# Kernel tuning notes

Hardware: AMD Instinct MI355X
Metric: run time of the kernel (lower is better)

Reference implementation:

```python
import jax, jax.numpy as jnp
import numpy as np

EPS = 1e-08


def setup_inputs() -> dict:
    key = jax.random.key(0)
    k1, k2, k3 = jax.random.split(key, 3)
    b, c, s = 4, 128, 32
    oc, k = 128, 3
    x = jax.random.normal(k1, (b, c, s, s, s), dtype=jnp.float32)
    y = jax.random.normal(k2, (b, c), dtype=jnp.float32)
    weight = jax.random.normal(k3, (oc, c, k, k, k), dtype=jnp.float32)
    return {"x": x, "y": y, "weight": weight}


def reference(x, y, weight):
    b, c, h, w, d = x.shape
    oc, ic, kh, kw, kd = weight.shape
    # modulate: per-sample scale of input channels
    ws = weight[None] * y[:, None, :, None, None, None]  # (b, oc, ic, k, k, k)
    # demodulate
    demod = jax.lax.rsqrt(jnp.sum(jnp.square(ws), axis=(2, 3, 4, 5)) + EPS)  # (b, oc)
    ws = ws * demod[:, :, None, None, None, None]
    # grouped conv: fold batch into channels, groups=b
    xr = x.reshape(1, b * c, h, w, d)
    wr = ws.reshape(b * oc, ic, kh, kw, kd)
    # same padding for stride=1, dilation=1: (k-1)//2
    pad = (kh - 1) // 2
    out = jax.lax.conv_general_dilated(
        xr, wr,
        window_strides=(1, 1, 1),
        padding=[(pad, pad)] * 3,
        feature_group_count=b,
        dimension_numbers=("NCDHW", "OIDHW", "NCDHW"),
    )
    return out.reshape(b, oc, h, w, d)
```

## Files before the change

kernel.cpp:

```cpp
#include <hip/hip_runtime.h>
#include <hip/hip_bf16.h>

typedef __attribute__((ext_vector_type(8))) short bf16x8;
typedef __attribute__((ext_vector_type(4))) float f32x4;
typedef unsigned short u16;
typedef unsigned int u32;

#define NP 34
#define XT_BYTES ((size_t)4 * NP * NP * NP * 128 * 2)

__device__ __forceinline__ u16 f2bf(float f) {
  __hip_bfloat16 h = __float2bfloat16(f);
  return __builtin_bit_cast(u16, h);
}

__device__ __forceinline__ void gload_lds16(const u16* g, u16* l) {
  __builtin_amdgcn_global_load_lds(
      (const __attribute__((address_space(1))) u32*)g,
      (__attribute__((address_space(3))) u32*)l, 16, 0, 0);
}

#define WAITV(N) asm volatile("s_waitcnt vmcnt(" #N ")" ::: "memory")
#define BAR() do { __builtin_amdgcn_s_barrier(); asm volatile("" ::: "memory"); } while (0)

__global__ __launch_bounds__(128) void kmodw(const float* __restrict__ w,
                                             const float* __restrict__ y,
                                             u16* __restrict__ wmod) {
  const int oc = blockIdx.x, b = blockIdx.y;
  const int ic = threadIdx.x;
  const float* wp = w + (oc * 128 + ic) * 27;
  float wv[27];
  float s = 0.f;
#pragma unroll
  for (int t = 0; t < 27; ++t) { wv[t] = wp[t]; s += wv[t] * wv[t]; }
  const float yv = y[b * 128 + ic];
  float v = yv * yv * s;
#pragma unroll
  for (int m = 1; m < 64; m <<= 1) v += __shfl_xor(v, m);
  __shared__ float part[2];
  const int lane = ic & 63, wid = ic >> 6;
  if (lane == 0) part[wid] = v;
  __syncthreads();
  const float demod = rsqrtf(part[0] + part[1] + 1e-8f);
  const float sc = yv * demod;
#pragma unroll
  for (int t = 0; t < 27; ++t)
    wmod[((b * 27 + t) * 128 + oc) * 128 + ic] = f2bf(wv[t] * sc);
}

__global__ __launch_bounds__(128) void khalo(u16* __restrict__ xt) {
  const int zy = blockIdx.x, b = blockIdx.y;
  const int zz = zy / NP, yy = zy % NP;
  u16* row = xt + ((size_t)((b * NP + zz) * NP + yy) * NP) * 128;
  u32* wp = (u32*)row;
  if (zz == 0 || zz == NP - 1 || yy == 0 || yy == NP - 1) {
#pragma unroll
    for (int i = 0; i < 17; ++i) wp[i * 128 + threadIdx.x] = 0;
  } else {
    if (threadIdx.x < 64) wp[threadIdx.x] = 0;
    else ((u32*)(row + 33 * 128))[threadIdx.x - 64] = 0;
  }
}

__global__ __launch_bounds__(256) void kcastx(const float* __restrict__ x,
                                              u16* __restrict__ xt) {
  const int yq = blockIdx.x, z = blockIdx.y, b = blockIdx.z;
  const int tid = threadIdx.x;
  __shared__ u16 t[32 * 132];
  const float* xp = x + (size_t)b * 128 * 32768 + (z * 32 + yq) * 32;
#pragma unroll
  for (int p = 0; p < 16; ++p) {
    const int ic = p * 8 + (tid >> 5), xx = tid & 31;
    t[xx * 132 + ic] = f2bf(xp[(size_t)ic * 32768 + xx]);
  }
  __syncthreads();
  u16* xtb = xt + (((size_t)(b * NP + z + 1) * NP + (yq + 1)) * NP + 1) * 128;
#pragma unroll
  for (int p = 0; p < 4; ++p) {
    const int xx = p * 8 + (tid >> 5), icq = tid & 31;
    *(ushort4*)(xtb + (size_t)xx * 128 + icq * 4) = *(const ushort4*)&t[xx * 132 + icq * 4];
  }
}

__global__ __launch_bounds__(256, 2) void kconv(const u16* __restrict__ xt,
                                                const u16* __restrict__ wmod,
                                                float* __restrict__ out) {
  __shared__ __align__(16) u16 Alds[2][128 * 64];
  __shared__ __align__(16) u16 Blds[2][160 * 64];
  const int tid = threadIdx.x;
  const int lane = tid & 63, wid = tid >> 6;
  const int bsw = ((blockIdx.x & 7) << 7) + (blockIdx.x >> 3);
  const int yt = bsw & 7, z = (bsw >> 3) & 31, b = bsw >> 8;
  const int y0 = yt << 2;
  const int wm = wid >> 1, wn = wid & 1;

  const u16* xb = xt + (size_t)b * (NP * NP * NP) * 128;
  const u16* wb = wmod + (size_t)b * 27 * 16384;

  f32x4 acc[4][4];
#pragma unroll
  for (int i = 0; i < 4; ++i)
#pragma unroll
    for (int j = 0; j < 4; ++j) acc[i][j] = (f32x4){0.f, 0.f, 0.f, 0.f};

  auto stageA = [&](int tap, int h) {
    const u16* base = wb + tap * 16384 + (h << 6);
#pragma unroll
    for (int k = 0; k < 4; ++k) {
      const int s = (k << 8) + tid;
      const int oc = s >> 3, j = s & 7;
      gload_lds16(base + (oc << 7) + ((j ^ (oc & 7)) << 3),
                  &Alds[h][((k << 8) + (wid << 6)) << 3]);
    }
  };
  auto stageB = [&](int g) {
    const int dz = g / 3 - 1, dy = g % 3 - 1;
    const int pz = z + 1 + dz;
#pragma unroll
    for (int k = 0; k < 10; ++k) {
      const int h = (k >= 5) ? 1 : 0;
      const int k5 = (k >= 5) ? (k - 5) : k;
      const int s = (k5 << 8) + tid;
      const int r = s >> 3, j = s & 7;
      const int yy = r / 40;
      int px = r - yy * 40;
      px = px < 34 ? px : 33;
      const int py = y0 + yy + 1 + dy;
      gload_lds16(xb + ((size_t)(pz * NP + py) * NP + px) * 128 + (h << 6) +
                      ((j ^ (r & 7)) << 3),
                  &Blds[h][((k5 << 8) + (wid << 6)) << 3]);
    }
  };

#define COMPHALF(H, DXI)                                                     \
  {                                                                          \
    const u16* Ah = &Alds[H][0];                                             \
    const u16* Bh = &Blds[H][0];                                             \
    _Pragma("unroll") for (int kk = 0; kk < 2; ++kk) {                       \
      const int sg = (kk << 2) + (lane >> 4);                                \
      bf16x8 af[4], bv[4];                                                   \
      _Pragma("unroll") for (int m = 0; m < 4; ++m) {                        \
        const int row = (wm << 6) + (m << 4) + (lane & 15);                  \
        af[m] = *(const bf16x8*)&Ah[(row << 6) + ((sg ^ (row & 7)) << 3)];   \
      }                                                                      \
      _Pragma("unroll") for (int n = 0; n < 4; ++n) {                        \
        const int nn = (wn << 6) + (n << 4) + (lane & 15);                   \
        const int r = ((nn >> 5) * 40) + (nn & 31) + (DXI);                  \
        bv[n] = *(const bf16x8*)&Bh[(r << 6) + ((sg ^ (r & 7)) << 3)];       \
      }                                                                      \
      __builtin_amdgcn_s_setprio(1);                                         \
      _Pragma("unroll") for (int m = 0; m < 4; ++m)                          \
        _Pragma("unroll") for (int n = 0; n < 4; ++n)                        \
          acc[m][n] = __builtin_amdgcn_mfma_f32_16x16x32_bf16(               \
              af[m], bv[n], acc[m][n], 0, 0, 0);                             \
      __builtin_amdgcn_s_setprio(0);                                         \
    }                                                                        \
  }

  stageB(0);
  stageA(0, 0);
  stageA(0, 1);

  for (int g = 0; g < 9; ++g) {
    const int t = g * 3;
    WAITV(4); BAR(); COMPHALF(0, 0); BAR(); stageA(t + 1, 0);
    WAITV(4); BAR(); COMPHALF(1, 0); BAR(); stageA(t + 1, 1);
    WAITV(4); BAR(); COMPHALF(0, 1); BAR(); stageA(t + 2, 0);
    WAITV(4); BAR(); COMPHALF(1, 1); BAR(); stageA(t + 2, 1);
    WAITV(4); BAR(); COMPHALF(0, 2); BAR();
    if (g < 8) stageA(t + 3, 0);
    if (g < 8) {
      WAITV(4); BAR(); COMPHALF(1, 2); BAR();
      stageB(g + 1);
      stageA(t + 3, 1);
    } else {
      WAITV(0); BAR(); COMPHALF(1, 2);
    }
  }

  const int col = lane & 15, rg = lane >> 4;
#pragma unroll
  for (int m = 0; m < 4; ++m) {
    const int ocb = (wm << 6) + (m << 4) + (rg << 2);
#pragma unroll
    for (int n = 0; n < 4; ++n) {
      const int nn = (wn << 6) + (n << 4) + col;
      const int yy = nn >> 5, xx = nn & 31;
      float* op = out + ((size_t)(b * 128 + ocb) << 15) + (z << 10) +
                  ((y0 + yy) << 5) + xx;
#pragma unroll
      for (int r = 0; r < 4; ++r) op[(size_t)r << 15] = acc[m][n][r];
    }
  }
#undef COMPHALF
}

extern "C" void kernel_launch(void* const* d_in, const int* in_sizes, int n_in,
                              void* d_out, int out_size, void* d_ws, size_t ws_size,
                              hipStream_t stream) {
  const float* x = (const float*)d_in[0];
  const float* y = (const float*)d_in[1];
  const float* w = (const float*)d_in[2];
  float* out = (float*)d_out;
  u16* xt = (u16*)d_ws;
  u16* wmod = (u16*)((char*)d_ws + XT_BYTES);

  hipLaunchKernelGGL(khalo, dim3(NP * NP, 4), dim3(128), 0, stream, xt);
  hipLaunchKernelGGL(kmodw, dim3(128, 4), dim3(128), 0, stream, w, y, wmod);
  hipLaunchKernelGGL(kcastx, dim3(32, 32, 4), dim3(256), 0, stream, x, xt);
  hipLaunchKernelGGL(kconv, dim3(1024), dim3(256), 0, stream, xt, wmod, out);
}
```

Before: 144.2 us.

## Load conv activations directly from global into registers with larger per-block tile

Drops LDS staging of the input (B) tile; each wave now loads its B fragments straight from global memory into registers, double-buffered across the two K halves of every tap. The block tile doubles to 128 oc by 256 spatial positions (8 y rows), each wave covers all 128 output channels, and the grid halves to 512 blocks. This removes the LDS traffic and barriers for B and reuses the weight tile across more positions. In exchange, accumulator registers double, B reuse across the three dx taps now depends on the cache instead of LDS, and global load latency sits directly on the compute path.

After: 160.4 us. 1.11x slower.

```diff
diff --git a/kernel.cpp b/kernel.cpp
--- a/kernel.cpp
+++ b/kernel.cpp
@@ -85,114 +85,110 @@
 __global__ __launch_bounds__(256, 2) void kconv(const u16* __restrict__ xt,
                                                 const u16* __restrict__ wmod,
                                                 float* __restrict__ out) {
-  __shared__ __align__(16) u16 Alds[2][128 * 64];
-  __shared__ __align__(16) u16 Blds[2][160 * 64];
+  __shared__ __align__(16) u16 Asm[2][1024 * 8];
   const int tid = threadIdx.x;
-  const int lane = tid & 63, wid = tid >> 6;
-  const int bsw = ((blockIdx.x & 7) << 7) + (blockIdx.x >> 3);
-  const int yt = bsw & 7, z = (bsw >> 3) & 31, b = bsw >> 8;
-  const int y0 = yt << 2;
-  const int wm = wid >> 1, wn = wid & 1;
-
-  const u16* xb = xt + (size_t)b * (NP * NP * NP) * 128;
+  const int lane = tid & 63, wn = tid >> 6;
+  const int l15 = lane & 15, sg = lane >> 4;
+  const int bsw = ((blockIdx.x & 7) << 6) + (blockIdx.x >> 3);
+  const int yt = bsw & 3, z = (bsw >> 2) & 31, b = bsw >> 7;
+  const int y0 = yt << 3;
+
   const u16* wb = wmod + (size_t)b * 27 * 16384;
-
-  f32x4 acc[4][4];
-#pragma unroll
-  for (int i = 0; i < 4; ++i)
+  const char* xbp = (const char*)(xt + (size_t)b * (NP * NP * NP) * 128);
+
+  int bofs[4];
+#pragma unroll
+  for (int nf = 0; nf < 4; ++nf) {
+    const int yy = (wn << 1) + (nf >> 1);
+    const int xx = ((nf & 1) << 4) + l15;
+    bofs[nf] = (((z + 1) * NP + (y0 + yy + 1)) * NP + (xx + 1)) * 256 + (sg << 4);
+  }
+
+  f32x4 acc[8][4];
+#pragma unroll
+  for (int i = 0; i < 8; ++i)
 #pragma unroll
     for (int j = 0; j < 4; ++j) acc[i][j] = (f32x4){0.f, 0.f, 0.f, 0.f};
 
   auto stageA = [&](int tap, int h) {
-    const u16* base = wb + tap * 16384 + (h << 6);
 #pragma unroll
     for (int k = 0; k < 4; ++k) {
       const int s = (k << 8) + tid;
-      const int oc = s >> 3, j = s & 7;
-      gload_lds16(base + (oc << 7) + ((j ^ (oc & 7)) << 3),
-                  &Alds[h][((k << 8) + (wid << 6)) << 3]);
+      const int oc = s >> 3, jp = s & 7, jg = jp ^ (oc & 7);
+      gload_lds16(wb + tap * 16384 + (oc << 7) + (h << 6) + (jg << 3),
+                  &Asm[h][s << 3]);
     }
   };
-  auto stageB = [&](int g) {
-    const int dz = g / 3 - 1, dy = g % 3 - 1;
-    const int pz = z + 1 + dz;
-#pragma unroll
-    for (int k = 0; k < 10; ++k) {
-      const int h = (k >= 5) ? 1 : 0;
-      const int k5 = (k >= 5) ? (k - 5) : k;
-      const int s = (k5 << 8) + tid;
-      const int r = s >> 3, j = s & 7;
-      const int yy = r / 40;
-      int px = r - yy * 40;
-      px = px < 34 ? px : 33;
-      const int py = y0 + yy + 1 + dy;
-      gload_lds16(xb + ((size_t)(pz * NP + py) * NP + px) * 128 + (h << 6) +
-                      ((j ^ (r & 7)) << 3),
-                  &Blds[h][((k5 << 8) + (wid << 6)) << 3]);
-    }
+  auto loadB = [&](bf16x8* bv, int toff) {
+#pragma unroll
+    for (int nf = 0; nf < 4; ++nf)
+#pragma unroll
+      for (int kk = 0; kk < 2; ++kk)
+        bv[nf * 2 + kk] =
+            *(const bf16x8*)(xbp + (bofs[nf] + toff + (kk << 6)));
   };
 
-#define COMPHALF(H, DXI)                                                     \
+#define COMPUTE(PAR, BV)                                                     \
   {                                                                          \
-    const u16* Ah = &Alds[H][0];                                             \
-    const u16* Bh = &Blds[H][0];                                             \
     _Pragma("unroll") for (int kk = 0; kk < 2; ++kk) {                       \
-      const int sg = (kk << 2) + (lane >> 4);                                \
-      bf16x8 af[4], bv[4];                                                   \
-      _Pragma("unroll") for (int m = 0; m < 4; ++m) {                        \
-        const int row = (wm << 6) + (m << 4) + (lane & 15);                  \
-        af[m] = *(const bf16x8*)&Ah[(row << 6) + ((sg ^ (row & 7)) << 3)];   \
-      }                                                                      \
-      _Pragma("unroll") for (int n = 0; n < 4; ++n) {                        \
-        const int nn = (wn << 6) + (n << 4) + (lane & 15);                   \
-        const int r = ((nn >> 5) * 40) + (nn & 31) + (DXI);                  \
-        bv[n] = *(const bf16x8*)&Bh[(r << 6) + ((sg ^ (r & 7)) << 3)];       \
+      bf16x8 af[8];                                                          \
+      _Pragma("unroll") for (int m = 0; m < 8; ++m) {                        \
+        const int oc = (m << 4) + l15;                                       \
+        const int jp = ((kk << 2) + sg) ^ (oc & 7);                          \
+        af[m] = *(const bf16x8*)&Asm[PAR][(oc << 6) + (jp << 3)];            \
       }                                                                      \
       __builtin_amdgcn_s_setprio(1);                                         \
-      _Pragma("unroll") for (int m = 0; m < 4; ++m)                          \
-        _Pragma("unroll") for (int n = 0; n < 4; ++n)                        \
-          acc[m][n] = __builtin_amdgcn_mfma_f32_16x16x32_bf16(               \
-              af[m], bv[n], acc[m][n], 0, 0, 0);                             \
+      _Pragma("unroll") for (int m = 0; m < 8; ++m)                          \
+        _Pragma("unroll") for (int nf = 0; nf < 4; ++nf)                     \
+          acc[m][nf] = __builtin_amdgcn_mfma_f32_16x16x32_bf16(              \
+              af[m], (BV)[nf * 2 + kk], acc[m][nf], 0, 0, 0);                \
       __builtin_amdgcn_s_setprio(0);                                         \
     }                                                                        \
   }
 
-  stageB(0);
+  bf16x8 bvE[8], bvO[8];
   stageA(0, 0);
   stageA(0, 1);
-
-  for (int g = 0; g < 9; ++g) {
-    const int t = g * 3;
-    WAITV(4); BAR(); COMPHALF(0, 0); BAR(); stageA(t + 1, 0);
-    WAITV(4); BAR(); COMPHALF(1, 0); BAR(); stageA(t + 1, 1);
-    WAITV(4); BAR(); COMPHALF(0, 1); BAR(); stageA(t + 2, 0);
-    WAITV(4); BAR(); COMPHALF(1, 1); BAR(); stageA(t + 2, 1);
-    WAITV(4); BAR(); COMPHALF(0, 2); BAR();
-    if (g < 8) stageA(t + 3, 0);
-    if (g < 8) {
-      WAITV(4); BAR(); COMPHALF(1, 2); BAR();
-      stageB(g + 1);
-      stageA(t + 3, 1);
-    } else {
-      WAITV(0); BAR(); COMPHALF(1, 2);
-    }
-  }
-
-  const int col = lane & 15, rg = lane >> 4;
-#pragma unroll
-  for (int m = 0; m < 4; ++m) {
-    const int ocb = (wm << 6) + (m << 4) + (rg << 2);
-#pragma unroll
-    for (int n = 0; n < 4; ++n) {
-      const int nn = (wn << 6) + (n << 4) + col;
-      const int yy = nn >> 5, xx = nn & 31;
+  {
+    const int t0 = ((-1 * NP - 1) * NP - 1) * 256;
+    loadB(bvE, t0);
+  }
+
+  for (int tap = 0; tap < 27; ++tap) {
+    const int dz = tap / 9 - 1, dy = (tap / 3) % 3 - 1, dx = tap % 3 - 1;
+    const int t0 = ((dz * NP + dy) * NP + dx) * 256;
+    const int tn = tap < 26 ? tap + 1 : 26;
+    const int dz2 = tn / 9 - 1, dy2 = (tn / 3) % 3 - 1, dx2 = tn % 3 - 1;
+    const int t1 = ((dz2 * NP + dy2) * NP + dx2) * 256;
+
+    WAITV(12); BAR();
+    loadB(bvO, t0 + 128);
+    COMPUTE(0, bvE);
+    BAR();
+    if (tap < 26) stageA(tap + 1, 0);
+
+    if (tap < 26) { WAITV(12); } else { WAITV(8); }
+    BAR();
+    loadB(bvE, t1);
+    COMPUTE(1, bvO);
+    BAR();
+    if (tap < 26) stageA(tap + 1, 1);
+  }
+
+#pragma unroll
+  for (int m = 0; m < 8; ++m) {
+    const int ocb = (m << 4) + (sg << 2);
+#pragma unroll
+    for (int nf = 0; nf < 4; ++nf) {
+      const int n = (wn << 6) + (nf << 4) + l15;
+      const int yy = n >> 5, xx = n & 31;
       float* op = out + ((size_t)(b * 128 + ocb) << 15) + (z << 10) +
                   ((y0 + yy) << 5) + xx;
 #pragma unroll
-      for (int r = 0; r < 4; ++r) op[(size_t)r << 15] = acc[m][n][r];
+      for (int r = 0; r < 4; ++r) op[(size_t)r << 15] = acc[m][nf][r];
     }
   }
-#undef COMPHALF
+#undef COMPUTE
 }
 
 extern "C" void kernel_launch(void* const* d_in, const int* in_sizes, int n_in,
@@ -208,5 +204,5 @@
   hipLaunchKernelGGL(khalo, dim3(NP * NP, 4), dim3(128), 0, stream, xt);
   hipLaunchKernelGGL(kmodw, dim3(128, 4), dim3(128), 0, stream, w, y, wmod);
   hipLaunchKernelGGL(kcastx, dim3(32, 32, 4), dim3(256), 0, stream, x, xt);
-  hipLaunchKernelGGL(kconv, dim3(1024), dim3(256), 0, stream, xt, wmod, out);
-}
+  hipLaunchKernelGGL(kconv, dim3(512), dim3(256), 0, stream, xt, wmod, out);
+}
```
